# Optimization experiments

Hardware: AMD Instinct MI355X
Metric: run time of the kernel (lower is better)

The kernel has to match this reference:

```python
import jax, jax.numpy as jnp
import numpy as np

B, S, D_IN, D_H = 4, 4096, 512, 64

def setup_inputs() -> dict:
    key = jax.random.key(0)
    ks = jax.random.split(key, 7)
    std = 1.0 / np.sqrt(D_IN)
    x = jax.random.normal(ks[0], (B, S, D_IN), dtype=jnp.float32)
    Wq = jax.random.uniform(ks[1], (D_IN, D_H), jnp.float32, -std, std)
    bq = jax.random.uniform(ks[2], (D_H,), jnp.float32, -std, std)
    Wk = jax.random.uniform(ks[3], (D_IN, D_H), jnp.float32, -std, std)
    bk = jax.random.uniform(ks[4], (D_H,), jnp.float32, -std, std)
    Wv = jax.random.uniform(ks[5], (D_IN, D_H), jnp.float32, -std, std)
    bv = jax.random.uniform(ks[6], (D_H,), jnp.float32, -std, std)
    return {"x": x, "Wq": Wq, "bq": bq, "Wk": Wk, "bk": bk, "Wv": Wv, "bv": bv}

def reference(x, Wq, bq, Wk, bk, Wv, bv):
    # q,k,v: [B, S, D_H]
    q = jnp.einsum('bsi,ih->bsh', x, Wq) + bq
    k = jnp.einsum('bsi,ih->bsh', x, Wk) + bk
    v = jnp.einsum('bsi,ih->bsh', x, Wv) + bv
    scale = 1.0 / jnp.sqrt(jnp.asarray(D_H, dtype=q.dtype))
    scores = jnp.einsum('bqh,bkh->bqk', q, k) * scale  # [B, S, S]
    att = jax.nn.softmax(scores, axis=-1)
    return jnp.einsum('bqk,bkh->bqh', att, v)
```

## Files before the change

### kernel.cpp

```cpp
#include <hip/hip_runtime.h>
#include <hip/hip_bf16.h>
#include <stdint.h>

#define LOG2E 1.4426950408889634f
#define SEQ 4096
#define DIN 512
#define DH 64
#define NSPLIT 8
#define QSCALE (0.125f * LOG2E)

typedef __attribute__((ext_vector_type(8))) short short8;
typedef __attribute__((ext_vector_type(16))) float f32x16;
typedef __attribute__((ext_vector_type(4))) float f32x4;

static __device__ __forceinline__ uint16_t f2bf(float f){
  uint32_t u = __float_as_uint(f);
  uint32_t r = u + 0x7fffu + ((u >> 16) & 1u);
  return (uint16_t)(r >> 16);
}

static __device__ __forceinline__ uint32_t cvt_pk_bf16(float lo, float hi){
  uint32_t d;
  asm("v_cvt_pk_bf16_f32 %0, %1, %2" : "=v"(d) : "v"(lo), "v"(hi));
  return d;
}

static __device__ __forceinline__ void perm32swap(uint32_t &a, uint32_t &b){
  asm("v_permlane32_swap_b32 %0, %1" : "+v"(a), "+v"(b));
}

static __device__ __forceinline__ float xadd32(float v){ return v + __shfl_xor(v, 32); }

static __device__ __forceinline__ void gload_lds16(const void* g, void* l){
  __builtin_amdgcn_global_load_lds(
      (const __attribute__((address_space(1))) unsigned int*)g,
      (__attribute__((address_space(3))) unsigned int*)l, 16, 0, 0);
}

__global__ void packw_kernel(const float* __restrict__ Wq, const float* __restrict__ Wk,
                             const float* __restrict__ Wv, uint4* __restrict__ Wp){
  int t0 = blockIdx.x * 256 + threadIdx.x;
  int lane = t0 & 63;
  int grp = t0 >> 6;
  int w3 = grp >> 6;
  int t  = (grp >> 2) & 15;
  int nc = grp & 3;
  const float* W = (w3 == 0) ? Wq : ((w3 == 1) ? Wk : Wv);
  int g = lane >> 4, cc = lane & 15;
  int k0 = t * 32 + g * 8;
  int n  = nc * 16 + cc;
  uint32_t o[4];
  #pragma unroll
  for (int p = 0; p < 4; ++p){
    float lo = W[(size_t)(k0 + 2*p    ) * DH + n];
    float hi = W[(size_t)(k0 + 2*p + 1) * DH + n];
    o[p] = cvt_pk_bf16(lo, hi);
  }
  Wp[(size_t)grp * 64 + lane] = make_uint4(o[0], o[1], o[2], o[3]);
}

__global__ __launch_bounds__(256, 4) void proj_kernel(
    const float* __restrict__ x, const uint4* __restrict__ Wp,
    const float* __restrict__ bq, const float* __restrict__ bk, const float* __restrict__ bv,
    uint16_t* __restrict__ Qs, uint16_t* __restrict__ Kb, uint16_t* __restrict__ Vt)
{
  int tid = threadIdx.x, lane = tid & 63, wv = tid >> 6;
  int c = lane & 15, g = lane >> 4;
  int rowbase = blockIdx.x * 16;

  f32x4 acc[3];
  #pragma unroll
  for (int j = 0; j < 3; ++j)
    #pragma unroll
    for (int r = 0; r < 4; ++r) acc[j][r] = 0.f;

  const float* xr = x + (size_t)(rowbase + c) * DIN;

  #pragma unroll 4
  for (int t = 0; t < 16; ++t){
    const float* p = xr + t * 32 + g * 8;
    float4 f0 = *(const float4*)(p);
    float4 f1 = *(const float4*)(p + 4);
    union { uint32_t u[4]; short8 s; } pk_;
    pk_.u[0] = cvt_pk_bf16(f0.x, f0.y);
    pk_.u[1] = cvt_pk_bf16(f0.z, f0.w);
    pk_.u[2] = cvt_pk_bf16(f1.x, f1.y);
    pk_.u[3] = cvt_pk_bf16(f1.z, f1.w);
    short8 xa = pk_.s;
    #pragma unroll
    for (int j = 0; j < 3; ++j){
      int i = wv * 3 + j;
      union { uint4 u; short8 s; } wf;
      wf.u = Wp[(size_t)((i >> 2) * 64 + t * 4 + (i & 3)) * 64 + lane];
      acc[j] = __builtin_amdgcn_mfma_f32_16x16x32_bf16(xa, wf.s, acc[j], 0, 0, 0);
    }
  }

  int mb0 = rowbase + 4 * g;
  #pragma unroll
  for (int j = 0; j < 3; ++j){
    int i = wv * 3 + j;
    int w3 = i >> 2, nc = i & 3, n = nc * 16 + c;
    const float* B = (w3 == 0) ? bq : ((w3 == 1) ? bk : bv);
    float bias = B[n];
    float v0 = acc[j][0] + bias;
    float v1 = acc[j][1] + bias;
    float v2 = acc[j][2] + bias;
    float v3 = acc[j][3] + bias;
    if (w3 == 0){
      Qs[(size_t)(mb0 + 0) * DH + n] = f2bf(v0 * QSCALE);
      Qs[(size_t)(mb0 + 1) * DH + n] = f2bf(v1 * QSCALE);
      Qs[(size_t)(mb0 + 2) * DH + n] = f2bf(v2 * QSCALE);
      Qs[(size_t)(mb0 + 3) * DH + n] = f2bf(v3 * QSCALE);
    } else if (w3 == 1){
      Kb[(size_t)(mb0 + 0) * DH + n] = f2bf(v0);
      Kb[(size_t)(mb0 + 1) * DH + n] = f2bf(v1);
      Kb[(size_t)(mb0 + 2) * DH + n] = f2bf(v2);
      Kb[(size_t)(mb0 + 3) * DH + n] = f2bf(v3);
    } else {
      int b = mb0 >> 12, mloc = mb0 & 4095;
      uint32_t lo = cvt_pk_bf16(v0, v1);
      uint32_t hi = cvt_pk_bf16(v2, v3);
      *(uint2*)(&Vt[((size_t)(b * DH + n)) * SEQ + mloc]) = make_uint2(lo, hi);
    }
  }
}

__global__ __launch_bounds__(256, 4) void attn_kernel(
    const uint16_t* __restrict__ Qs, const uint16_t* __restrict__ Kb,
    const uint16_t* __restrict__ Vt, uint16_t* __restrict__ Pacc,
    float* __restrict__ Pl)
{
  __shared__ uint8_t lds[32768];
  const int tid = threadIdx.x, lane = tid & 63, wv = tid >> 6;
  const int bid = blockIdx.x;
  const int split = bid & 7, batch = (bid >> 3) & 3, qtile = bid >> 5;
  const int c = lane & 31, hi = lane >> 5;
  const int NT = SEQ / NSPLIT / 64;

  const int qrow = batch * SEQ + qtile * 128 + wv * 32 + c;

  short8 qf[4];
  {
    const uint16_t* qp = Qs + (size_t)qrow * DH;
    #pragma unroll
    for (int ks = 0; ks < 4; ++ks){
      union { uint4 u; short8 s; } v;
      v.u = *(const uint4*)(qp + ks * 16 + hi * 8);
      qf[ks] = v.s;
    }
  }

  int addr8[2][4];
  #pragma unroll
  for (int a = 0; a < 2; ++a)
    #pragma unroll
    for (int b = 0; b < 4; ++b)
      addr8[a][b] = (32 * a + c) * 128 + (((2 * b + hi) ^ (c & 7)) << 4);

  const int slotA = wv * 128 + lane, slotB = slotA + 64;
  const int keyA = slotA >> 3, keyB = slotB >> 3;
  const int dgA = (slotA & 7) ^ (keyA & 7), dgB = (slotB & 7) ^ (keyB & 7);
  const uint8_t* Kg = (const uint8_t*)Kb + ((size_t)(batch * SEQ + split * 512)) * (DH * 2);
  const uint8_t* KgA = Kg + keyA * 128 + dgA * 16;
  const uint8_t* KgB = Kg + keyB * 128 + dgB * 16;
  const uint8_t* Vg = (const uint8_t*)Vt + (size_t)batch * (DH * SEQ * 2) + split * 1024;
  const uint8_t* VgA = Vg + keyA * (SEQ * 2) + dgA * 16;
  const uint8_t* VgB = Vg + keyB * (SEQ * 2) + dgB * 16;

  f32x16 acc[2];
  #pragma unroll
  for (int d = 0; d < 2; ++d)
    #pragma unroll
    for (int r = 0; r < 16; ++r) acc[d][r] = 0.f;

  f32x16 ZERO;
  #pragma unroll
  for (int r = 0; r < 16; ++r) ZERO[r] = 0.f;
  asm volatile("" : "+v"(ZERO));

  float l0_ = 0.f, l1_ = 0.f, l2_ = 0.f, l3_ = 0.f;

  gload_lds16(KgA, lds + wv * 2048);
  gload_lds16(KgB, lds + wv * 2048 + 1024);
  gload_lds16(VgA, lds + 8192 + wv * 2048);
  gload_lds16(VgB, lds + 8192 + wv * 2048 + 1024);
  __syncthreads();

  #pragma unroll 1
  for (int t = 0; t < NT; ++t){
    const int OFF = (t & 1) << 14;
    const int NOFF = OFF ^ 16384;

    if (t < NT - 1){
      gload_lds16(KgA + (size_t)(t + 1) * 8192, lds + NOFF + wv * 2048);
      gload_lds16(KgB + (size_t)(t + 1) * 8192, lds + NOFF + wv * 2048 + 1024);
      gload_lds16(VgA + (size_t)(t + 1) * 128,  lds + NOFF + 8192 + wv * 2048);
      gload_lds16(VgB + (size_t)(t + 1) * 128,  lds + NOFF + 8192 + wv * 2048 + 1024);
    }

    f32x16 sa[2];
    __builtin_amdgcn_s_setprio(1);
    #pragma unroll
    for (int st = 0; st < 2; ++st){
      #pragma unroll
      for (int ks = 0; ks < 4; ++ks){
        short8 kf = *(const short8*)(lds + OFF + addr8[st][ks]);
        sa[st] = __builtin_amdgcn_mfma_f32_32x32x16_bf16(
            kf, qf[ks], (ks == 0) ? ZERO : sa[st], 0, 0, 0);
      }
    }
    __builtin_amdgcn_s_setprio(0);

    uint32_t pk[2][8];
    #pragma unroll
    for (int st = 0; st < 2; ++st){
      float pv[16];
      #pragma unroll
      for (int r = 0; r < 16; ++r) pv[r] = __builtin_amdgcn_exp2f(sa[st][r]);
      #pragma unroll
      for (int r = 0; r < 4; ++r){
        l0_ += pv[4 * r + 0];
        l1_ += pv[4 * r + 1];
        l2_ += pv[4 * r + 2];
        l3_ += pv[4 * r + 3];
      }
      #pragma unroll
      for (int p = 0; p < 8; ++p) pk[st][p] = cvt_pk_bf16(pv[2 * p], pv[2 * p + 1]);
    }

    short8 pf[4];
    #pragma unroll
    for (int kslab = 0; kslab < 4; ++kslab){
      int st = kslab >> 1, q4 = (kslab & 1) * 4;
      uint32_t w_[4];
      #pragma unroll
      for (int w1 = 0; w1 < 2; ++w1){
        uint32_t a = pk[st][q4 + w1];
        uint32_t b = pk[st][q4 + 2 + w1];
        perm32swap(a, b);
        w_[w1] = a; w_[2 + w1] = b;
      }
      union { uint32_t u[4]; short8 s; } u_;
      u_.u[0] = w_[0]; u_.u[1] = w_[1]; u_.u[2] = w_[2]; u_.u[3] = w_[3];
      pf[kslab] = u_.s;
    }

    __builtin_amdgcn_s_setprio(1);
    #pragma unroll
    for (int kslab = 0; kslab < 4; ++kslab){
      #pragma unroll
      for (int dst = 0; dst < 2; ++dst){
        short8 vf = *(const short8*)(lds + OFF + 8192 + addr8[dst][kslab]);
        acc[dst] = __builtin_amdgcn_mfma_f32_32x32x16_bf16(vf, pf[kslab], acc[dst], 0, 0, 0);
      }
    }
    __builtin_amdgcn_s_setprio(0);

    __syncthreads();
  }

  uint16_t* pa = Pacc + ((size_t)split * 16384 + qrow) * DH;
  #pragma unroll
  for (int dst = 0; dst < 2; ++dst)
    #pragma unroll
    for (int rq = 0; rq < 4; ++rq){
      uint32_t lo = cvt_pk_bf16(acc[dst][rq * 4 + 0], acc[dst][rq * 4 + 1]);
      uint32_t hi2 = cvt_pk_bf16(acc[dst][rq * 4 + 2], acc[dst][rq * 4 + 3]);
      *(uint2*)(pa + dst * 32 + rq * 8 + hi * 4) = make_uint2(lo, hi2);
    }
  float l_tot = xadd32((l0_ + l1_) + (l2_ + l3_));
  if (hi == 0) Pl[(size_t)split * 16384 + qrow] = l_tot;
}

__global__ __launch_bounds__(256) void combine_kernel(
    const uint16_t* __restrict__ Pacc, const float* __restrict__ Pl,
    float* __restrict__ out)
{
  int t = blockIdx.x * 256 + threadIdx.x;
  int q = t >> 3, part = t & 7;
  float l = 0.f;
  #pragma unroll
  for (int s = 0; s < NSPLIT; ++s) l += Pl[(size_t)s * 16384 + q];
  float inv = 1.0f / l;

  float o[8];
  #pragma unroll
  for (int i = 0; i < 8; ++i) o[i] = 0.f;
  #pragma unroll
  for (int s = 0; s < NSPLIT; ++s){
    const uint16_t* p = Pacc + ((size_t)s * 16384 + q) * DH + part * 8;
    uint4 v = *(const uint4*)(p);
    const uint32_t* w = (const uint32_t*)&v;
    #pragma unroll
    for (int k = 0; k < 4; ++k){
      o[2 * k + 0] += __uint_as_float((w[k] & 0xffffu) << 16);
      o[2 * k + 1] += __uint_as_float((w[k] >> 16) << 16);
    }
  }
  float* ob = out + (size_t)q * DH + part * 8;
  #pragma unroll
  for (int i = 0; i < 2; ++i){
    float4 v = make_float4(o[4*i] * inv, o[4*i+1] * inv, o[4*i+2] * inv, o[4*i+3] * inv);
    *(float4*)(ob + 4 * i) = v;
  }
}

extern "C" void kernel_launch(void* const* d_in, const int* in_sizes, int n_in,
                              void* d_out, int out_size, void* d_ws, size_t ws_size,
                              hipStream_t stream)
{
  (void)in_sizes; (void)n_in; (void)out_size; (void)ws_size;
  const float* x  = (const float*)d_in[0];
  const float* Wq = (const float*)d_in[1];
  const float* bq = (const float*)d_in[2];
  const float* Wk = (const float*)d_in[3];
  const float* bk = (const float*)d_in[4];
  const float* Wv = (const float*)d_in[5];
  const float* bv = (const float*)d_in[6];
  float* out = (float*)d_out;
  uint8_t* ws = (uint8_t*)d_ws;

  const size_t o_Wp = 0;
  const size_t o_Q  = 196608;
  const size_t o_K  = o_Q + 2097152;
  const size_t o_Vt = o_K + 2097152;
  const size_t o_Pa = o_Vt + 2097152;
  const size_t o_Pl = o_Pa + 16777216;

  packw_kernel<<<48, 256, 0, stream>>>(Wq, Wk, Wv, (uint4*)(ws + o_Wp));
  proj_kernel<<<1024, 256, 0, stream>>>(x, (const uint4*)(ws + o_Wp), bq, bk, bv,
      (uint16_t*)(ws + o_Q), (uint16_t*)(ws + o_K), (uint16_t*)(ws + o_Vt));
  attn_kernel<<<1024, 256, 0, stream>>>((const uint16_t*)(ws + o_Q), (const uint16_t*)(ws + o_K),
      (const uint16_t*)(ws + o_Vt), (uint16_t*)(ws + o_Pa), (float*)(ws + o_Pl));
  combine_kernel<<<512, 256, 0, stream>>>((const uint16_t*)(ws + o_Pa), (const float*)(ws + o_Pl), out);
}
```

Baseline: 66.04 us.

## Stage x tile in LDS for projection, relax attn occupancy, widen combine grid

```diff
diff --git a/kernel.cpp b/kernel.cpp
--- a/kernel.cpp
+++ b/kernel.cpp
@@ -64,29 +64,39 @@
     const float* __restrict__ bq, const float* __restrict__ bk, const float* __restrict__ bv,
     uint16_t* __restrict__ Qs, uint16_t* __restrict__ Kb, uint16_t* __restrict__ Vt)
 {
+  __shared__ uint16_t xl[16][520];
   int tid = threadIdx.x, lane = tid & 63, wv = tid >> 6;
   int c = lane & 15, g = lane >> 4;
   int rowbase = blockIdx.x * 16;
 
+  {
+    int row = tid >> 4, cb = (tid & 15) * 32;
+    const float* src = x + (size_t)(rowbase + row) * DIN + cb;
+    #pragma unroll
+    for (int i = 0; i < 2; ++i){
+      float4 f0 = *(const float4*)(src + i * 16 + 0);
+      float4 f1 = *(const float4*)(src + i * 16 + 4);
+      float4 f2 = *(const float4*)(src + i * 16 + 8);
+      float4 f3 = *(const float4*)(src + i * 16 + 12);
+      uint4 w0 = make_uint4(cvt_pk_bf16(f0.x, f0.y), cvt_pk_bf16(f0.z, f0.w),
+                            cvt_pk_bf16(f1.x, f1.y), cvt_pk_bf16(f1.z, f1.w));
+      uint4 w1 = make_uint4(cvt_pk_bf16(f2.x, f2.y), cvt_pk_bf16(f2.z, f2.w),
+                            cvt_pk_bf16(f3.x, f3.y), cvt_pk_bf16(f3.z, f3.w));
+      *(uint4*)(&xl[row][cb + i * 16]) = w0;
+      *(uint4*)(&xl[row][cb + i * 16 + 8]) = w1;
+    }
+  }
+  __syncthreads();
+
   f32x4 acc[3];
   #pragma unroll
   for (int j = 0; j < 3; ++j)
     #pragma unroll
     for (int r = 0; r < 4; ++r) acc[j][r] = 0.f;
-
-  const float* xr = x + (size_t)(rowbase + c) * DIN;
 
   #pragma unroll 4
   for (int t = 0; t < 16; ++t){
-    const float* p = xr + t * 32 + g * 8;
-    float4 f0 = *(const float4*)(p);
-    float4 f1 = *(const float4*)(p + 4);
-    union { uint32_t u[4]; short8 s; } pk_;
-    pk_.u[0] = cvt_pk_bf16(f0.x, f0.y);
-    pk_.u[1] = cvt_pk_bf16(f0.z, f0.w);
-    pk_.u[2] = cvt_pk_bf16(f1.x, f1.y);
-    pk_.u[3] = cvt_pk_bf16(f1.z, f1.w);
-    short8 xa = pk_.s;
+    short8 xa = *(const short8*)(&xl[c][t * 32 + g * 8]);
     #pragma unroll
     for (int j = 0; j < 3; ++j){
       int i = wv * 3 + j;
@@ -126,7 +136,7 @@
   }
 }
 
-__global__ __launch_bounds__(256, 4) void attn_kernel(
+__global__ __launch_bounds__(256, 3) void attn_kernel(
     const uint16_t* __restrict__ Qs, const uint16_t* __restrict__ Kb,
     const uint16_t* __restrict__ Vt, uint16_t* __restrict__ Pacc,
     float* __restrict__ Pl)
@@ -278,32 +288,26 @@
     float* __restrict__ out)
 {
   int t = blockIdx.x * 256 + threadIdx.x;
-  int q = t >> 3, part = t & 7;
+  int q = t >> 4, part = t & 15;
   float l = 0.f;
   #pragma unroll
   for (int s = 0; s < NSPLIT; ++s) l += Pl[(size_t)s * 16384 + q];
   float inv = 1.0f / l;
 
-  float o[8];
-  #pragma unroll
-  for (int i = 0; i < 8; ++i) o[i] = 0.f;
+  float o[4];
+  #pragma unroll
+  for (int i = 0; i < 4; ++i) o[i] = 0.f;
   #pragma unroll
   for (int s = 0; s < NSPLIT; ++s){
-    const uint16_t* p = Pacc + ((size_t)s * 16384 + q) * DH + part * 8;
-    uint4 v = *(const uint4*)(p);
-    const uint32_t* w = (const uint32_t*)&v;
-    #pragma unroll
-    for (int k = 0; k < 4; ++k){
-      o[2 * k + 0] += __uint_as_float((w[k] & 0xffffu) << 16);
-      o[2 * k + 1] += __uint_as_float((w[k] >> 16) << 16);
-    }
-  }
-  float* ob = out + (size_t)q * DH + part * 8;
-  #pragma unroll
-  for (int i = 0; i < 2; ++i){
-    float4 v = make_float4(o[4*i] * inv, o[4*i+1] * inv, o[4*i+2] * inv, o[4*i+3] * inv);
-    *(float4*)(ob + 4 * i) = v;
-  }
+    const uint16_t* p = Pacc + ((size_t)s * 16384 + q) * DH + part * 4;
+    uint2 v = *(const uint2*)(p);
+    o[0] += __uint_as_float((v.x & 0xffffu) << 16);
+    o[1] += __uint_as_float((v.x >> 16) << 16);
+    o[2] += __uint_as_float((v.y & 0xffffu) << 16);
+    o[3] += __uint_as_float((v.y >> 16) << 16);
+  }
+  float4 v = make_float4(o[0] * inv, o[1] * inv, o[2] * inv, o[3] * inv);
+  *(float4*)(out + (size_t)q * DH + part * 4) = v;
 }
 
 extern "C" void kernel_launch(void* const* d_in, const int* in_sizes, int n_in,
@@ -333,5 +337,5 @@
       (uint16_t*)(ws + o_Q), (uint16_t*)(ws + o_K), (uint16_t*)(ws + o_Vt));
   attn_kernel<<<1024, 256, 0, stream>>>((const uint16_t*)(ws + o_Q), (const uint16_t*)(ws + o_K),
       (const uint16_t*)(ws + o_Vt), (uint16_t*)(ws + o_Pa), (float*)(ws + o_Pl));
-  combine_kernel<<<512, 256, 0, stream>>>((const uint16_t*)(ws + o_Pa), (const float*)(ws + o_Pl), out);
-}
+  combine_kernel<<<1024, 256, 0, stream>>>((const uint16_t*)(ws + o_Pa), (const float*)(ws + o_Pl), out);
+}
```

New measurement: 53.38 us (median of 2 runs). 19.2% less time.
